# Performance work log

Hardware: AMD Instinct MI355X
Metric: run time of the kernel (lower is better)

The kernel has to match this reference:

```python
import jax, jax.numpy as jnp
import numpy as np

_PHI = (1.0 + 5.0 ** 0.5) / 2.0
_VS = np.array([[0, 1, _PHI], [0, 1, -_PHI], [0, -1, _PHI], [0, -1, -_PHI],
                [1, _PHI, 0], [1, -_PHI, 0], [-1, _PHI, 0], [-1, -_PHI, 0],
                [_PHI, 0, 1], [_PHI, 0, -1], [-_PHI, 0, 1], [-_PHI, 0, -1]], dtype=np.float32)
_VS = _VS / np.linalg.norm(_VS, axis=-1, keepdims=True)  # 12 icosahedron vertices
_COLOR_COM = np.array([(0, 1, 2, 3, 4, 5), (0, 5, 4, 3, 2, 1), (2, 5, 4, 1, 0, 3), (5, 0, 1, 3, 2, 4),
                       (3, 5, 2, 0, 4, 1), (4, 0, 5, 2, 1, 3), (1, 3, 4, 2, 0, 5), (1, 0, 2, 4, 3, 5),
                       (4, 1, 2, 5, 0, 3), (3, 1, 4, 0, 2, 5), (5, 1, 0, 4, 2, 3), (2, 4, 5, 3, 0, 1)])
_INV = np.argsort(_COLOR_COM, axis=-1)  # inverse perms: scatter_(-1, color_com, W) == gather with _INV
_C2V = np.array([(0, 1), (6, 7), (2, 11), (4, 9), (5, 8), (3, 10)])
_ROLL = np.array([(0, 1, 2, 3, 4, 5), (0, 2, 3, 4, 5, 1), (0, 3, 4, 5, 1, 2), (0, 4, 5, 1, 2, 3), (0, 5, 1, 2, 3, 4)])
_HEADS = 8


def _build_sym(Wp):
    """(..., 18) raw params -> (..., 13, 12, 6) symmetry-expanded weights."""
    lead = Wp.shape[:-1]
    top = jnp.concatenate([Wp[..., 0:1], jnp.repeat(Wp[..., 1:2], 5, axis=-1)], axis=-1)[..., None, :]
    bot = jnp.concatenate([Wp[..., 2:3], jnp.repeat(Wp[..., 3:4], 5, axis=-1)], axis=-1)[..., None, :]
    cen = jnp.concatenate([Wp[..., 4:5], jnp.repeat(Wp[..., 5:6], 5, axis=-1)], axis=-1)[..., None, :]
    sym = Wp[..., 6:18].reshape(lead + (2, 6))[..., _ROLL].reshape(lead + (10, 6))
    W13 = jnp.concatenate([top, bot, sym, cen], axis=-2)  # (..., 13, 6)
    return W13[..., _INV]  # (..., 13, 12, 6): rotated copies via inverse color permutations


def setup_inputs() -> dict:
    key = jax.random.key(0)
    ks = jax.random.split(key, 6)
    bs, V, n, di, do = 1, 2048, 16, 32, 64
    s = 0.05
    return {
        "neighbor_index": jax.random.randint(ks[0], (bs, V, n), 0, V),
        "vertices": jax.random.normal(ks[1], (bs, V, 3), dtype=jnp.float32),
        "feature_map": jax.random.normal(ks[2], (bs, di, V, 6), dtype=jnp.float32),
        "W_dim": jax.random.normal(ks[3], (di + 1, di), dtype=jnp.float32) * s,
        "W": jax.random.normal(ks[4], (do, di, 18), dtype=jnp.float32) * s,
        "W_dir": jax.random.normal(ks[5], (di * _HEADS, 18), dtype=jnp.float32) * s,
    }


def reference(neighbor_index, vertices, feature_map, W_dim, W, W_dir):
    bs, V, n = neighbor_index.shape
    do, di, _ = W.shape
    H = _HEADS
    dph = di // H
    vs = jnp.asarray(_VS)
    c2v = jnp.asarray(_C2V)
    # neighbor direction (normalized)
    neigh = jax.vmap(lambda v, idx: v[idx])(vertices, neighbor_index)  # (bs,V,n,3)
    nd = neigh - vertices[:, :, None, :]
    ndn = nd / jnp.maximum(jnp.linalg.norm(nd, axis=-1, keepdims=True), 1e-12)
    # symmetry-expanded weights
    W_ro = _build_sym(W)       # (do, di, 13, 12, 6)
    Wd_ro = _build_sym(W_dir)  # (di*H, 13, 12, 6)
    # gather neighbor features: (bs, di, V, n, 6)
    nf = jax.vmap(lambda fm, idx: fm[:, idx])(feature_map, neighbor_index)
    # direction features discretized onto the 6 color axes
    de = jnp.einsum('vi,bqni->bqnv', vs, ndn)          # (bs,V,n,12)
    de = de[..., c2v].max(axis=-1)                      # (bs,V,n,6)
    cross = jnp.concatenate([nf, de[:, None]], axis=1)  # (bs, di+1, V, n, 6)
    cross = jnp.einsum('co,bcpni->bopni', W_dim, cross)  # (bs, di, V, n, 6)
    # per-head attention over neighbors
    Wdr = Wd_ro.reshape(H, di, 13, 12, 6).transpose(0, 1, 2, 4, 3)  # (h, c, k, i, r)
    act = jnp.einsum('hckir,bcpni->hbkpnr', Wdr[:, :, :12], cross) / (dph ** 0.5)
    act = jax.nn.softmax(act, axis=-2)                  # softmax over neighbors n
    cross_h = cross.reshape(bs, H, dph, V, n, 6)
    nfm = jnp.einsum('hbkpnr,bhcpni->bhckpir', act, cross_h).reshape(bs, di, 12, V, 6, 12)
    feat = jnp.einsum('dckri,bckpir->bdkpr', W_ro[:, :, :12], nfm)   # (bs,do,12,V,12)
    center = jnp.einsum('dcri,bcpi->bdpr', W_ro[:, :, 12], feature_map)  # (bs,do,V,12)
    ka = feat.sum(axis=2) + center                       # (bs,do,V,12)
    ka = ka[..., c2v].max(axis=-1)                       # (bs,do,V,6)
    return (ka, feature_map)
```

## Files before the change

kernel.cpp:

```cpp
#include <hip/hip_runtime.h>
#include <cstdint>
#include <cstddef>

#define NN 16
#define DI 32
#define DO 64

typedef short bf16x8 __attribute__((ext_vector_type(8)));
typedef float f32x4 __attribute__((ext_vector_type(4)));

__device__ __constant__ int c_INV[12][6] = {
  {0,1,2,3,4,5},{0,5,4,3,2,1},{4,3,0,5,2,1},{1,2,4,3,5,0},
  {3,5,2,0,4,1},{1,4,3,5,0,2},{4,0,3,1,2,5},{1,0,2,4,3,5},
  {4,1,2,5,0,3},{3,1,4,0,2,5},{2,1,4,5,3,0},{4,5,0,3,1,2}};
__device__ __constant__ int c_ROLL[5][6] = {
  {0,1,2,3,4,5},{0,2,3,4,5,1},{0,3,4,5,1,2},{0,4,5,1,2,3},{0,5,1,2,3,4}};
__device__ __constant__ float c_VS[12][3] = {
  {0.f, 0.5257311121f, 0.8506508084f},
  {0.f, 0.5257311121f, -0.8506508084f},
  {0.f, -0.5257311121f, 0.8506508084f},
  {0.f, -0.5257311121f, -0.8506508084f},
  {0.5257311121f, 0.8506508084f, 0.f},
  {0.5257311121f, -0.8506508084f, 0.f},
  {-0.5257311121f, 0.8506508084f, 0.f},
  {-0.5257311121f, -0.8506508084f, 0.f},
  {0.8506508084f, 0.f, 0.5257311121f},
  {0.8506508084f, 0.f, -0.5257311121f},
  {-0.8506508084f, 0.f, 0.5257311121f},
  {-0.8506508084f, 0.f, -0.5257311121f}};
__device__ __constant__ int c_C2V[6][2] = {{0,1},{6,7},{2,11},{4,9},{5,8},{3,10}};

__device__ inline unsigned short f2bf(float f) {
  unsigned int u = __float_as_uint(f);
  unsigned int r = (u + 0x7fffu + ((u >> 16) & 1u)) >> 16;
  return (unsigned short)r;
}
__device__ inline float bf2f(unsigned short h) {
  return __uint_as_float(((unsigned int)h) << 16);
}
__device__ inline unsigned int pack2(float a, float b) {
  return (unsigned int)f2bf(a) | ((unsigned int)f2bf(b) << 16);
}

__device__ inline float sym13(const float* __restrict__ w, int k, int j) {
  if (k == 0)  return w[j == 0 ? 0 : 1];
  if (k == 1)  return w[j == 0 ? 2 : 3];
  if (k == 12) return w[j == 0 ? 4 : 5];
  int a = (k - 2) / 5, rr = (k - 2) % 5;
  return w[6 + a * 6 + c_ROLL[rr][j]];
}

__global__ __launch_bounds__(256) void k0_expand(
    const float* __restrict__ W, const float* __restrict__ Wdir,
    const float* __restrict__ fm,
    unsigned short* __restrict__ A_bf,
    unsigned short* __restrict__ W2k,
    unsigned short* __restrict__ Wck,
    unsigned short* __restrict__ fmTbf,
    float* __restrict__ out_fm, int V) {
  int idx = blockIdx.x * 256 + threadIdx.x;
  if (idx < 221184) {
    int row = idx / 192, ci = idx % 192;
    int h = row / 144, k = (row / 12) % 12, r = row % 12;
    int c = ci / 6, i = ci % 6;
    int rt = row >> 4, rl = row & 15;
    int ks = ci >> 5, q = (ci >> 3) & 3, j = ci & 7;
    A_bf[(((rt * 6 + ks) * 4 + q) * 16 + rl) * 8 + j] =
        f2bf(0.5f * sym13(&Wdir[(h * 32 + c) * 18], k, c_INV[r][i]));
  } else if (idx < 1990656) {
    int e = idx - 221184;
    int kr = e / 12288, rem = e % 12288;
    int k = kr / 12, r = kr % 12, d = rem / 192, ci = rem % 192;
    int c = ci / 6, i = ci % 6;
    int ks = ci >> 5, q = (ci >> 3) & 3, j = ci & 7;
    W2k[kr * 12288 + ((ks * 4 + q) * 64 + d) * 8 + j] =
        f2bf(sym13(&W[(d * 32 + c) * 18], k, c_INV[r][i]));
  } else if (idx < 2138112) {
    int e = idx - 1990656;
    int r = e / 12288, rem = e % 12288, d = rem / 192, ci = rem % 192;
    int c = ci / 6, i = ci % 6;
    int ks = ci >> 5, q = (ci >> 3) & 3, j = ci & 7;
    Wck[r * 12288 + ((ks * 4 + q) * 64 + d) * 8 + j] =
        f2bf(sym13(&W[(d * 32 + c) * 18], 12, c_INV[r][i]));
  } else {
    int e = idx - 2138112;
    if (e < 192 * V) {
      int p = e / 192, ci = e % 192, c = ci / 6, i = ci % 6;
      float v = fm[(c * V + p) * 6 + i];
      fmTbf[e] = f2bf(v);
      out_fm[(c * V + p) * 6 + i] = v;
    }
  }
}

__global__ __launch_bounds__(256) void k1_cross(
    const int* __restrict__ nbi, const float* __restrict__ verts,
    const float* __restrict__ fm, const float* __restrict__ Wdim,
    unsigned short* __restrict__ cross_n,
    unsigned short* __restrict__ crossT_g, int V) {
  __shared__ float in_s[NN * 33 * 6];
  __shared__ float wd_s[33 * 32];
  __shared__ unsigned int cross_u[1536];
  __shared__ int nb_s[NN];
  int p = blockIdx.x, t = threadIdx.x;
  if (t < NN) nb_s[t] = nbi[p * NN + t];
  for (int idx = t; idx < 1056; idx += 256) wd_s[idx] = Wdim[idx];
  __syncthreads();
  for (int idx = t; idx < NN * 32 * 6; idx += 256) {
    int n = idx / 192, rest = idx % 192, c = rest / 6, i = rest % 6;
    in_s[(n * 33 + c) * 6 + i] = fm[(c * V + nb_s[n]) * 6 + i];
  }
  if (t < NN) {
    int n = t, nb = nb_s[n];
    float px = verts[p * 3 + 0], py = verts[p * 3 + 1], pz = verts[p * 3 + 2];
    float dx = verts[nb * 3 + 0] - px, dy = verts[nb * 3 + 1] - py, dz = verts[nb * 3 + 2] - pz;
    float L = sqrtf(dx * dx + dy * dy + dz * dz);
    float inv = 1.0f / fmaxf(L, 1e-12f);
    dx *= inv; dy *= inv; dz *= inv;
    float de[12];
    #pragma unroll
    for (int v = 0; v < 12; ++v)
      de[v] = c_VS[v][0] * dx + c_VS[v][1] * dy + c_VS[v][2] * dz;
    #pragma unroll
    for (int j = 0; j < 6; ++j)
      in_s[(n * 33 + 32) * 6 + j] = fmaxf(de[c_C2V[j][0]], de[c_C2V[j][1]]);
  }
  __syncthreads();
  for (int idx = t; idx < 1536; idx += 256) {
    int n = idx / 96, cp2 = idx % 96;
    int ci0 = cp2 * 2, ci1 = ci0 + 1;
    int o0 = ci0 / 6, i0 = ci0 % 6;
    int o1 = ci1 / 6, i1 = ci1 % 6;
    float s0 = 0.f, s1 = 0.f;
    #pragma unroll
    for (int c = 0; c <= 32; ++c) {
      float f0 = in_s[(n * 33 + c) * 6 + i0];
      float f1 = in_s[(n * 33 + c) * 6 + i1];
      s0 = fmaf(wd_s[c * 32 + o0], f0, s0);
      s1 = fmaf(wd_s[c * 32 + o1], f1, s1);
    }
    cross_u[idx] = (unsigned int)f2bf(s0) | ((unsigned int)f2bf(s1) << 16);
  }
  __syncthreads();
  {
    const uint4* src = (const uint4*)cross_u;
    uint4* d1 = (uint4*)(cross_n + (size_t)p * 3072);
    for (int idx = t; idx < 384; idx += 256) d1[idx] = src[idx];
  }
  {
    unsigned int* d2 = (unsigned int*)(crossT_g + (size_t)p * 3072);
    for (int idx = t; idx < 1536; idx += 256) {
      int np = idx / 192, ci = idx % 192;
      unsigned int u0 = cross_u[(2 * np) * 96 + (ci >> 1)];
      unsigned int u1 = cross_u[(2 * np + 1) * 96 + (ci >> 1)];
      unsigned int h0 = (ci & 1) ? (u0 >> 16) : (u0 & 0xffffu);
      unsigned int h1 = (ci & 1) ? (u1 & 0xffff0000u) : (u1 << 16);
      d2[ci * 8 + np] = h0 | h1;
    }
  }
}

__global__ __launch_bounds__(256, 4) void k2_main(
    const unsigned short* __restrict__ A_bf,
    const unsigned short* __restrict__ cross_n,
    const unsigned short* __restrict__ crossT_g,
    unsigned short* __restrict__ nfm, int V) {
  __shared__ __align__(16) unsigned short crossT[2][192][40];
  int t = threadIdx.x;
  int w = t >> 6, lane = t & 63;
  int quad = lane >> 4, col = lane & 15;
  int p0 = blockIdx.x * 2;

  bf16x8 Afr[2][6];
  #pragma unroll
  for (int p = 0; p < 2; ++p)
    #pragma unroll
    for (int ks = 0; ks < 6; ++ks)
      Afr[p][ks] = *(const bf16x8*)(cross_n + (size_t)(p0 + p) * 3072 + col * 192 + ks * 32 + quad * 8);

  for (int idx = t; idx < 768; idx += 256) {
    int p = idx / 384, rem = idx % 384, ci = rem >> 1, half = rem & 1;
    *(uint4*)&crossT[p][ci][half * 8] =
        *(const uint4*)(crossT_g + (size_t)(p0 + p) * 3072 + ci * 16 + half * 8);
  }
  for (int idx = t; idx < 768; idx += 256) {
    int p = idx / 384, rem = idx % 384, ci = rem >> 1, half = rem & 1;
    *(uint4*)&crossT[p][ci][16 + half * 8] = make_uint4(0u, 0u, 0u, 0u);
  }
  __syncthreads();

  int s0l = quad * 32 + col;
  int s1l = s0l + 16;

  for (int rt = w; rt < 72; rt += 4) {
    int h = rt / 9;
    int krbase = rt * 16 - h * 144;
    f32x4 acc[2];
    acc[0] = (f32x4){0.f, 0.f, 0.f, 0.f};
    acc[1] = (f32x4){0.f, 0.f, 0.f, 0.f};
    const unsigned short* Abase = A_bf + rt * 3072 + quad * 128 + col * 8;
    #pragma unroll
    for (int ks = 0; ks < 6; ++ks) {
      bf16x8 wf = *(const bf16x8*)(Abase + ks * 512);
      acc[0] = __builtin_amdgcn_mfma_f32_16x16x32_bf16(Afr[0][ks], wf, acc[0], 0, 0, 0);
      acc[1] = __builtin_amdgcn_mfma_f32_16x16x32_bf16(Afr[1][ks], wf, acc[1], 0, 0, 0);
    }
    int row0 = h * 24 + col;
    int row1 = min(h * 24 + 16 + col, 191);
    #pragma unroll
    for (int p = 0; p < 2; ++p) {
      float v0 = acc[p][0], v1 = acc[p][1], v2 = acc[p][2], v3 = acc[p][3];
      float mx = fmaxf(fmaxf(v0, v1), fmaxf(v2, v3));
      mx = fmaxf(mx, __shfl_xor(mx, 16));
      mx = fmaxf(mx, __shfl_xor(mx, 32));
      float e0 = __expf(v0 - mx), e1 = __expf(v1 - mx);
      float e2 = __expf(v2 - mx), e3 = __expf(v3 - mx);
      float s = (e0 + e1) + (e2 + e3);
      s += __shfl_xor(s, 16);
      s += __shfl_xor(s, 32);
      float inv = __builtin_amdgcn_rcpf(s);
      unsigned int lo = pack2(e0 * inv, e1 * inv);
      unsigned int hi = pack2(e2 * inv, e3 * inv);
      unsigned int b0 = (unsigned int)__shfl((int)lo, s0l);
      unsigned int b1 = (unsigned int)__shfl((int)hi, s0l);
      unsigned int b2 = (unsigned int)__shfl((int)lo, s1l);
      unsigned int b3 = (unsigned int)__shfl((int)hi, s1l);
      bool vq = (quad < 2);
      union { uint4 u; bf16x8 v; } cvt;
      cvt.u = make_uint4(vq ? b0 : 0u, vq ? b1 : 0u, vq ? b2 : 0u, vq ? b3 : 0u);
      bf16x8 bv = cvt.v;
      bf16x8 a0 = *(const bf16x8*)&crossT[p][row0][quad * 8];
      bf16x8 a1 = *(const bf16x8*)&crossT[p][row1][quad * 8];
      f32x4 o0 = (f32x4){0.f, 0.f, 0.f, 0.f}, o1 = o0;
      o0 = __builtin_amdgcn_mfma_f32_16x16x32_bf16(a0, bv, o0, 0, 0, 0);
      o1 = __builtin_amdgcn_mfma_f32_16x16x32_bf16(a1, bv, o1, 0, 0, 0);
      size_t rowbase = (((size_t)(p0 + p) * 8 + h) * 144 + krbase + col) * 24;
      uint2 w0;
      w0.x = pack2(o0[0], o0[1]);
      w0.y = pack2(o0[2], o0[3]);
      *(uint2*)(nfm + rowbase + quad * 4) = w0;
      if (quad < 2) {
        uint2 w1;
        w1.x = pack2(o1[0], o1[1]);
        w1.y = pack2(o1[2], o1[3]);
        *(uint2*)(nfm + rowbase + 16 + quad * 4) = w1;
      }
    }
  }
}

__global__ __launch_bounds__(256) void k3_feat(
    const unsigned short* __restrict__ W2k,
    const unsigned short* __restrict__ Wck,
    const unsigned short* __restrict__ fmTbf,
    const unsigned short* __restrict__ nfm,
    float* __restrict__ ka12, int V) {
  __shared__ float red[3][32][64];
  int pb = blockIdx.x, r = blockIdx.y;
  int t = threadIdx.x, w = t >> 6, lane = t & 63;
  int quad = lane >> 4, col = lane & 15;
  int p0 = pb * 32;
  f32x4 acc[4][2];
  #pragma unroll
  for (int m = 0; m < 4; ++m)
    #pragma unroll
    for (int j = 0; j < 2; ++j) acc[m][j] = (f32x4){0.f, 0.f, 0.f, 0.f};

  int base24[6];
  #pragma unroll
  for (int ks = 0; ks < 6; ++ks) {
    int ci = ks * 32 + quad * 8;
    int hh = ci / 24, oo = ci - hh * 24;
    base24[ks] = hh * 3456 + oo;
  }

  const unsigned short* Bn0 = nfm + (size_t)(p0 + col) * 27648;
  const unsigned short* Bn1 = nfm + (size_t)(p0 + 16 + col) * 27648;
  const unsigned short* Bc0 = fmTbf + (size_t)(p0 + col) * 192;
  const unsigned short* Bc1 = fmTbf + (size_t)(p0 + 16 + col) * 192;

  int nkb = (w == 3) ? 4 : 3;
  for (int i = 0; i < nkb; ++i) {
    int kb = w * 3 + i;
    const unsigned short* Ab;
    int kr24 = 0;
    if (kb < 12) { Ab = W2k + (size_t)(kb * 12 + r) * 12288; kr24 = (kb * 12 + r) * 24; }
    else         { Ab = Wck + (size_t)r * 12288; }
    const unsigned short* Albase = Ab + quad * 512 + col * 8;
    #pragma unroll
    for (int ks = 0; ks < 6; ++ks) {
      bf16x8 b0, b1;
      if (kb < 12) {
        b0 = *(const bf16x8*)(Bn0 + base24[ks] + kr24);
        b1 = *(const bf16x8*)(Bn1 + base24[ks] + kr24);
      } else {
        int ko = ks * 32 + quad * 8;
        b0 = *(const bf16x8*)(Bc0 + ko);
        b1 = *(const bf16x8*)(Bc1 + ko);
      }
      #pragma unroll
      for (int m = 0; m < 4; ++m) {
        bf16x8 a = *(const bf16x8*)(Albase + ks * 2048 + m * 128);
        acc[m][0] = __builtin_amdgcn_mfma_f32_16x16x32_bf16(a, b0, acc[m][0], 0, 0, 0);
        acc[m][1] = __builtin_amdgcn_mfma_f32_16x16x32_bf16(a, b1, acc[m][1], 0, 0, 0);
      }
    }
  }
  if (w > 0) {
    #pragma unroll
    for (int m = 0; m < 4; ++m)
      #pragma unroll
      for (int j = 0; j < 2; ++j)
        #pragma unroll
        for (int rr = 0; rr < 4; ++rr)
          red[w - 1][m * 8 + j * 4 + rr][lane] = acc[m][j][rr];
  }
  __syncthreads();
  if (w == 0) {
    #pragma unroll
    for (int m = 0; m < 4; ++m)
      #pragma unroll
      for (int j = 0; j < 2; ++j)
        #pragma unroll
        for (int rr = 0; rr < 4; ++rr) {
          int ri = m * 8 + j * 4 + rr;
          acc[m][j][rr] += red[0][ri][lane] + red[1][ri][lane] + red[2][ri][lane];
        }
    #pragma unroll
    for (int m = 0; m < 4; ++m) {
      #pragma unroll
      for (int rr = 0; rr < 4; ++rr) {
        int d = m * 16 + quad * 4 + rr;
        float* dst = &ka12[(size_t)(r * 64 + d) * V + p0 + col];
        dst[0]  = acc[m][0][rr];
        dst[16] = acc[m][1][rr];
      }
    }
  }
}

__global__ __launch_bounds__(256) void k4_final(
    const float* __restrict__ ka12, float* __restrict__ out, int V) {
  int idx = blockIdx.x * 256 + threadIdx.x;
  int total = DO * V * 6;
  if (idx >= total) return;
  int j = idx % 6, rem = idx / 6;
  int p = rem % V, d = rem / V;
  size_t base = (size_t)d * V + p;
  float a = ka12[(size_t)c_C2V[j][0] * 64 * V + base];
  float b = ka12[(size_t)c_C2V[j][1] * 64 * V + base];
  out[idx] = fmaxf(a, b);
}

extern "C" void kernel_launch(void* const* d_in, const int* in_sizes, int n_in,
                              void* d_out, int out_size, void* d_ws, size_t ws_size,
                              hipStream_t stream) {
  const int* nbi = (const int*)d_in[0];
  const float* verts = (const float*)d_in[1];
  const float* fm = (const float*)d_in[2];
  const float* Wdim = (const float*)d_in[3];
  const float* W = (const float*)d_in[4];
  const float* Wdir = (const float*)d_in[5];
  float* out = (float*)d_out;
  float* ws = (float*)d_ws;
  int V = in_sizes[0] / NN;

  unsigned short* A_bf  = (unsigned short*)ws;
  unsigned short* W2k   = (unsigned short*)(ws + 110592);
  unsigned short* Wck   = (unsigned short*)(ws + 995328);
  unsigned short* fmTbf = (unsigned short*)(ws + 1069056);
  size_t o = 1069056 + (size_t)96 * V;
  unsigned short* cross_n = (unsigned short*)(ws + o);
  o += (size_t)1536 * V;
  unsigned short* crossT_g = (unsigned short*)(ws + o);
  o += (size_t)1536 * V;
  float* ka12 = ws + o;
  o += (size_t)768 * V;
  unsigned short* nfm = (unsigned short*)(ws + o);

  int n0 = 2138112 + 192 * V;
  k0_expand<<<(n0 + 255) / 256, 256, 0, stream>>>(W, Wdir, fm, A_bf, W2k, Wck, fmTbf,
                                                  out + (size_t)DO * V * 6, V);
  k1_cross<<<V, 256, 0, stream>>>(nbi, verts, fm, Wdim, cross_n, crossT_g, V);
  k2_main<<<V / 2, 256, 0, stream>>>(A_bf, cross_n, crossT_g, nfm, V);
  k3_feat<<<dim3(V / 32, 12), 256, 0, stream>>>(W2k, Wck, fmTbf, nfm, ka12, V);
  k4_final<<<(DO * V * 6 + 255) / 256, 256, 0, stream>>>(ka12, out, V);
}
```

Measured before the change: 186.9 us.

## Fuse color-axis max into feature GEMM, use K16 MFMA, vectorize gather

The k4 max-over-vertex-pair pass is folded into k3: each 512-thread block computes both rotations of a color axis in two wave-halves and takes the max in shared memory before writing the output directly. This drops the ka12 intermediate buffer and one kernel launch. In k2, the attention-weighted MFMA switches to a 16x16x16 bf16 instruction when it is available, which avoids the cross-lane shuffles and zero-padded K=32 operand. k1's neighbor feature gather is vectorized to float2 loads. The trade-offs are larger blocks with more shared memory in k3, and the shuffle-free K16 path depending on the compiler exposing that builtin.

New measurement: 191.2 us. 2.3% more time.

```diff
diff --git a/kernel.cpp b/kernel.cpp
--- a/kernel.cpp
+++ b/kernel.cpp
@@ -7,7 +7,18 @@
 #define DO 64
 
 typedef short bf16x8 __attribute__((ext_vector_type(8)));
+typedef short bf16x4 __attribute__((ext_vector_type(4)));
 typedef float f32x4 __attribute__((ext_vector_type(4)));
+
+#if defined(__has_builtin)
+#  if __has_builtin(__builtin_amdgcn_mfma_f32_16x16x16_bf16)
+#    define MFMA_K16(a, b, c) __builtin_amdgcn_mfma_f32_16x16x16_bf16(a, b, c, 0, 0, 0)
+#    define HAVE_K16 1
+#  elif __has_builtin(__builtin_amdgcn_mfma_f32_16x16x16bf16_1k)
+#    define MFMA_K16(a, b, c) __builtin_amdgcn_mfma_f32_16x16x16bf16_1k(a, b, c, 0, 0, 0)
+#    define HAVE_K16 1
+#  endif
+#endif
 
 __device__ __constant__ int c_INV[12][6] = {
   {0,1,2,3,4,5},{0,5,4,3,2,1},{4,3,0,5,2,1},{1,2,4,3,5,0},
@@ -106,9 +117,14 @@
   if (t < NN) nb_s[t] = nbi[p * NN + t];
   for (int idx = t; idx < 1056; idx += 256) wd_s[idx] = Wdim[idx];
   __syncthreads();
-  for (int idx = t; idx < NN * 32 * 6; idx += 256) {
-    int n = idx / 192, rest = idx % 192, c = rest / 6, i = rest % 6;
-    in_s[(n * 33 + c) * 6 + i] = fm[(c * V + nb_s[n]) * 6 + i];
+  for (int idx = t; idx < NN * 32; idx += 256) {
+    int n = idx >> 5, c = idx & 31;
+    const float* src = fm + ((size_t)c * V + nb_s[n]) * 6;
+    float2 a  = *(const float2*)(src + 0);
+    float2 b  = *(const float2*)(src + 2);
+    float2 cd = *(const float2*)(src + 4);
+    float* d = &in_s[(n * 33 + c) * 6];
+    d[0] = a.x; d[1] = a.y; d[2] = b.x; d[3] = b.y; d[4] = cd.x; d[5] = cd.y;
   }
   if (t < NN) {
     int n = t, nb = nb_s[n];
@@ -189,12 +205,13 @@
   }
   __syncthreads();
 
+#ifndef HAVE_K16
   int s0l = quad * 32 + col;
   int s1l = s0l + 16;
+#endif
 
   for (int rt = w; rt < 72; rt += 4) {
     int h = rt / 9;
-    int krbase = rt * 16 - h * 144;
     f32x4 acc[2];
     acc[0] = (f32x4){0.f, 0.f, 0.f, 0.f};
     acc[1] = (f32x4){0.f, 0.f, 0.f, 0.f};
@@ -221,6 +238,15 @@
       float inv = __builtin_amdgcn_rcpf(s);
       unsigned int lo = pack2(e0 * inv, e1 * inv);
       unsigned int hi = pack2(e2 * inv, e3 * inv);
+      f32x4 o0 = (f32x4){0.f, 0.f, 0.f, 0.f}, o1 = o0;
+#ifdef HAVE_K16
+      union { uint2 u; bf16x4 v; } bcvt;
+      bcvt.u = make_uint2(lo, hi);
+      bf16x4 a0 = *(const bf16x4*)&crossT[p][row0][quad * 4];
+      bf16x4 a1 = *(const bf16x4*)&crossT[p][row1][quad * 4];
+      o0 = MFMA_K16(a0, bcvt.v, o0);
+      o1 = MFMA_K16(a1, bcvt.v, o1);
+#else
       unsigned int b0 = (unsigned int)__shfl((int)lo, s0l);
       unsigned int b1 = (unsigned int)__shfl((int)hi, s0l);
       unsigned int b2 = (unsigned int)__shfl((int)lo, s1l);
@@ -228,13 +254,12 @@
       bool vq = (quad < 2);
       union { uint4 u; bf16x8 v; } cvt;
       cvt.u = make_uint4(vq ? b0 : 0u, vq ? b1 : 0u, vq ? b2 : 0u, vq ? b3 : 0u);
-      bf16x8 bv = cvt.v;
       bf16x8 a0 = *(const bf16x8*)&crossT[p][row0][quad * 8];
       bf16x8 a1 = *(const bf16x8*)&crossT[p][row1][quad * 8];
-      f32x4 o0 = (f32x4){0.f, 0.f, 0.f, 0.f}, o1 = o0;
-      o0 = __builtin_amdgcn_mfma_f32_16x16x32_bf16(a0, bv, o0, 0, 0, 0);
-      o1 = __builtin_amdgcn_mfma_f32_16x16x32_bf16(a1, bv, o1, 0, 0, 0);
-      size_t rowbase = (((size_t)(p0 + p) * 8 + h) * 144 + krbase + col) * 24;
+      o0 = __builtin_amdgcn_mfma_f32_16x16x32_bf16(a0, cvt.v, o0, 0, 0, 0);
+      o1 = __builtin_amdgcn_mfma_f32_16x16x32_bf16(a1, cvt.v, o1, 0, 0, 0);
+#endif
+      size_t rowbase = (size_t)(p0 + p) * 27648 + (size_t)(rt * 16 + col) * 24;
       uint2 w0;
       w0.x = pack2(o0[0], o0[1]);
       w0.y = pack2(o0[2], o0[3]);
@@ -249,22 +274,24 @@
   }
 }
 
-__global__ __launch_bounds__(256) void k3_feat(
+__global__ __launch_bounds__(512) void k3_feat(
     const unsigned short* __restrict__ W2k,
     const unsigned short* __restrict__ Wck,
     const unsigned short* __restrict__ fmTbf,
     const unsigned short* __restrict__ nfm,
-    float* __restrict__ ka12, int V) {
-  __shared__ float red[3][32][64];
-  int pb = blockIdx.x, r = blockIdx.y;
+    float* __restrict__ out, int V) {
+  __shared__ float red[2][3][32][64];
+  int pb = blockIdx.x, j = blockIdx.y;
   int t = threadIdx.x, w = t >> 6, lane = t & 63;
+  int rhalf = w >> 2, kw = w & 3;
+  int r = c_C2V[j][rhalf];
   int quad = lane >> 4, col = lane & 15;
   int p0 = pb * 32;
   f32x4 acc[4][2];
   #pragma unroll
   for (int m = 0; m < 4; ++m)
     #pragma unroll
-    for (int j = 0; j < 2; ++j) acc[m][j] = (f32x4){0.f, 0.f, 0.f, 0.f};
+    for (int jj = 0; jj < 2; ++jj) acc[m][jj] = (f32x4){0.f, 0.f, 0.f, 0.f};
 
   int base24[6];
   #pragma unroll
@@ -279,9 +306,9 @@
   const unsigned short* Bc0 = fmTbf + (size_t)(p0 + col) * 192;
   const unsigned short* Bc1 = fmTbf + (size_t)(p0 + 16 + col) * 192;
 
-  int nkb = (w == 3) ? 4 : 3;
+  int nkb = (kw == 3) ? 4 : 3;
   for (int i = 0; i < nkb; ++i) {
-    int kb = w * 3 + i;
+    int kb = kw * 3 + i;
     const unsigned short* Ab;
     int kr24 = 0;
     if (kb < 12) { Ab = W2k + (size_t)(kb * 12 + r) * 12288; kr24 = (kb * 12 + r) * 24; }
@@ -306,50 +333,50 @@
       }
     }
   }
-  if (w > 0) {
+  if (kw > 0) {
     #pragma unroll
     for (int m = 0; m < 4; ++m)
       #pragma unroll
-      for (int j = 0; j < 2; ++j)
+      for (int jj = 0; jj < 2; ++jj)
         #pragma unroll
         for (int rr = 0; rr < 4; ++rr)
-          red[w - 1][m * 8 + j * 4 + rr][lane] = acc[m][j][rr];
-  }
-  __syncthreads();
-  if (w == 0) {
+          red[rhalf][kw - 1][m * 8 + jj * 4 + rr][lane] = acc[m][jj][rr];
+  }
+  __syncthreads();
+  if (kw == 0) {
     #pragma unroll
     for (int m = 0; m < 4; ++m)
       #pragma unroll
-      for (int j = 0; j < 2; ++j)
+      for (int jj = 0; jj < 2; ++jj)
         #pragma unroll
         for (int rr = 0; rr < 4; ++rr) {
-          int ri = m * 8 + j * 4 + rr;
-          acc[m][j][rr] += red[0][ri][lane] + red[1][ri][lane] + red[2][ri][lane];
+          int ri = m * 8 + jj * 4 + rr;
+          acc[m][jj][rr] += red[rhalf][0][ri][lane] + red[rhalf][1][ri][lane] + red[rhalf][2][ri][lane];
         }
-    #pragma unroll
-    for (int m = 0; m < 4; ++m) {
+  }
+  if (w == 4) {
+    #pragma unroll
+    for (int m = 0; m < 4; ++m)
       #pragma unroll
-      for (int rr = 0; rr < 4; ++rr) {
-        int d = m * 16 + quad * 4 + rr;
-        float* dst = &ka12[(size_t)(r * 64 + d) * V + p0 + col];
-        dst[0]  = acc[m][0][rr];
-        dst[16] = acc[m][1][rr];
-      }
-    }
-  }
-}
-
-__global__ __launch_bounds__(256) void k4_final(
-    const float* __restrict__ ka12, float* __restrict__ out, int V) {
-  int idx = blockIdx.x * 256 + threadIdx.x;
-  int total = DO * V * 6;
-  if (idx >= total) return;
-  int j = idx % 6, rem = idx / 6;
-  int p = rem % V, d = rem / V;
-  size_t base = (size_t)d * V + p;
-  float a = ka12[(size_t)c_C2V[j][0] * 64 * V + base];
-  float b = ka12[(size_t)c_C2V[j][1] * 64 * V + base];
-  out[idx] = fmaxf(a, b);
+      for (int jj = 0; jj < 2; ++jj)
+        #pragma unroll
+        for (int rr = 0; rr < 4; ++rr)
+          red[1][0][m * 8 + jj * 4 + rr][lane] = acc[m][jj][rr];
+  }
+  __syncthreads();
+  if (w == 0) {
+    #pragma unroll
+    for (int m = 0; m < 4; ++m)
+      #pragma unroll
+      for (int jj = 0; jj < 2; ++jj)
+        #pragma unroll
+        for (int rr = 0; rr < 4; ++rr) {
+          float v = fmaxf(acc[m][jj][rr], red[1][0][m * 8 + jj * 4 + rr][lane]);
+          int d = m * 16 + quad * 4 + rr;
+          int p = p0 + jj * 16 + col;
+          out[((size_t)d * V + p) * 6 + j] = v;
+        }
+  }
 }
 
 extern "C" void kernel_launch(void* const* d_in, const int* in_sizes, int n_in,
@@ -374,8 +401,6 @@
   o += (size_t)1536 * V;
   unsigned short* crossT_g = (unsigned short*)(ws + o);
   o += (size_t)1536 * V;
-  float* ka12 = ws + o;
-  o += (size_t)768 * V;
   unsigned short* nfm = (unsigned short*)(ws + o);
 
   int n0 = 2138112 + 192 * V;
@@ -383,6 +408,5 @@
                                                   out + (size_t)DO * V * 6, V);
   k1_cross<<<V, 256, 0, stream>>>(nbi, verts, fm, Wdim, cross_n, crossT_g, V);
   k2_main<<<V / 2, 256, 0, stream>>>(A_bf, cross_n, crossT_g, nfm, V);
-  k3_feat<<<dim3(V / 32, 12), 256, 0, stream>>>(W2k, Wck, fmTbf, nfm, ka12, V);
-  k4_final<<<(DO * V * 6 + 255) / 256, 256, 0, stream>>>(ka12, out, V);
-}
+  k3_feat<<<dim3(V / 32, 6), 512, 0, stream>>>(W2k, Wck, fmTbf, nfm, out, V);
+}
```
